# Performance work log

Hardware: AMD Instinct MI355X
Metric: run time of the kernel (lower is better)

## Reference

```python
import jax, jax.numpy as jnp
import numpy as np


def setup_inputs() -> dict:
    key = jax.random.key(0)
    k1, k2, k3 = jax.random.split(key, 3)
    B, H, S, D = 4, 16, 2048, 64
    q = jax.random.normal(k1, (B, H, S, D), dtype=jnp.float32)
    k = jax.random.normal(k2, (B, H, S, D), dtype=jnp.float32)
    v = jax.random.normal(k3, (B, H, S, D), dtype=jnp.float32)
    mask = jnp.ones((B, 1, 1, S), dtype=jnp.int32)  # broadcastable key mask
    return {"q": q, "k": k, "v": v, "mask": mask, "dropout": 0}


def reference(q, k, v, mask, dropout):
    # scores: [B, H, Sq, Sk]
    head_size = q.shape[-1]
    scale = 1.0 / np.sqrt(head_size).astype(np.float32)
    scores = jnp.einsum('bhqd,bhkd->bhqk', q, k) * scale
    scores = jnp.where(mask == 0, jnp.float32(-1e9), scores)
    weights = jax.nn.softmax(scores, axis=-1)
    # dropout is identity in deterministic/eval reference
    values = jnp.einsum('bhqk,bhkd->bhqd', weights, v)
    return values
```

## Files before the change

kernel.cpp:

```cpp
#include <hip/hip_runtime.h>
#include <hip/hip_bf16.h>


#define S_LEN 2048
#define D_DIM 64
#define KVB   64
#define QB    128
#define LDK   72

typedef float  f32x16 __attribute__((ext_vector_type(16)));
typedef __bf16 bf8    __attribute__((ext_vector_type(8)));
typedef __bf16 bf4    __attribute__((ext_vector_type(4)));
typedef __bf16 bf2    __attribute__((ext_vector_type(2)));
typedef unsigned int u32x4 __attribute__((ext_vector_type(4)));

__global__ __launch_bounds__(256, 3)
void sdpa_kernel(const float* __restrict__ q, const float* __restrict__ k,
                 const float* __restrict__ v, const int* __restrict__ mask,
                 float* __restrict__ out) {
    const int bh   = blockIdx.x;
    const int qt   = blockIdx.y;
    const int b    = bh >> 4;
    const int tid  = threadIdx.x;
    const int wave = tid >> 6;
    const int lane = tid & 63;
    const int l31  = lane & 31;
    const int hi   = lane >> 5;

    __shared__ __bf16 Kl[64 * LDK];
    __shared__ __bf16 Vt[64 * LDK];

    const size_t base = (size_t)bh * (S_LEN * D_DIM);

    const int qrow = qt * QB + wave * 32 + l31;
    bf8 qf[4];
    {
        const float* qp = q + base + (size_t)qrow * D_DIM;
        #pragma unroll
        for (int ds = 0; ds < 4; ++ds) {
            float4 a = *(const float4*)(qp + ds * 16 + hi * 8);
            float4 c = *(const float4*)(qp + ds * 16 + hi * 8 + 4);
            bf8 f;
            f[0] = (__bf16)(a.x * 0.125f); f[1] = (__bf16)(a.y * 0.125f);
            f[2] = (__bf16)(a.z * 0.125f); f[3] = (__bf16)(a.w * 0.125f);
            f[4] = (__bf16)(c.x * 0.125f); f[5] = (__bf16)(c.y * 0.125f);
            f[6] = (__bf16)(c.z * 0.125f); f[7] = (__bf16)(c.w * 0.125f);
            qf[ds] = f;
        }
    }

    f32x16 acc0 = (f32x16)0.0f;
    f32x16 acc1 = (f32x16)0.0f;
    float mrun = -INFINITY, lrun = 0.0f;

    for (int kv0 = 0; kv0 < S_LEN; kv0 += KVB) {
        __syncthreads();
        {
            int colg = (tid & 15) * 4;
            int row0 = tid >> 4;
            #pragma unroll
            for (int pp = 0; pp < 4; ++pp) {
                int row = row0 + pp * 16;
                float4 x = *(const float4*)(k + base + (size_t)(kv0 + row) * D_DIM + colg);
                bf4 s;
                s[0] = (__bf16)x.x; s[1] = (__bf16)x.y; s[2] = (__bf16)x.z; s[3] = (__bf16)x.w;
                *(bf4*)(&Kl[row * LDK + colg]) = s;
            }
        }
        {
            int d  = tid & 63;
            int kg = (tid >> 6) * 16;
            __bf16 tmp[16];
            #pragma unroll
            for (int j = 0; j < 16; ++j)
                tmp[j] = (__bf16)v[base + (size_t)(kv0 + kg + j) * D_DIM + d];
            *(bf8*)(&Vt[d * LDK + kg])     = *(bf8*)(&tmp[0]);
            *(bf8*)(&Vt[d * LDK + kg + 8]) = *(bf8*)(&tmp[8]);
        }
        __syncthreads();

        unsigned long long bm = __ballot(mask[b * S_LEN + kv0 + lane] != 0);

        f32x16 p0 = (f32x16)0.0f, p1 = (f32x16)0.0f;
        #pragma unroll
        for (int ds = 0; ds < 4; ++ds) {
            bf8 k0 = *(const bf8*)(&Kl[l31 * LDK        + ds * 16 + hi * 8]);
            bf8 k1 = *(const bf8*)(&Kl[(32 + l31) * LDK + ds * 16 + hi * 8]);
            p0 = __builtin_amdgcn_mfma_f32_32x32x16_bf16(k0, qf[ds], p0, 0, 0, 0);
            p1 = __builtin_amdgcn_mfma_f32_32x32x16_bf16(k1, qf[ds], p1, 0, 0, 0);
        }

        if (bm != ~0ull) {
            #pragma unroll
            for (int r = 0; r < 16; ++r) {
                int kr = (r & 3) + 8 * (r >> 2) + 4 * hi;
                if (!((bm >> kr) & 1))        p0[r] = -1e9f;
                if (!((bm >> (32 + kr)) & 1)) p1[r] = -1e9f;
            }
        }

        float mx = -INFINITY;
        #pragma unroll
        for (int r = 0; r < 16; ++r) mx = fmaxf(mx, fmaxf(p0[r], p1[r]));
        mx = fmaxf(mx, __shfl_xor(mx, 32));
        float mnew = fmaxf(mrun, mx);
        float sc = __expf(mrun - mnew);
        mrun = mnew;
        lrun *= sc;
        #pragma unroll
        for (int r = 0; r < 16; ++r) { acc0[r] *= sc; acc1[r] *= sc; }

        float rs = 0.0f;
        auto do_kb = [&](f32x16& p, int kbbase) {
            #pragma unroll
            for (int r = 0; r < 16; ++r) { p[r] = __expf(p[r] - mnew); rs += p[r]; }
            unsigned wds[8], xw[8];
            #pragma unroll
            for (int j = 0; j < 8; ++j) {
                bf2 t; t[0] = (__bf16)p[2 * j]; t[1] = (__bf16)p[2 * j + 1];
                wds[j] = __builtin_bit_cast(unsigned, t);
            }
            #pragma unroll
            for (int j = 0; j < 8; ++j)
                xw[j] = (unsigned)__shfl_xor((int)wds[j], 32);
            #pragma unroll
            for (int ks = 0; ks < 2; ++ks) {
                u32x4 uu;
                uu[0] = hi ? xw[4 * ks + 2]  : wds[4 * ks + 0];
                uu[1] = hi ? xw[4 * ks + 3]  : wds[4 * ks + 1];
                uu[2] = hi ? wds[4 * ks + 2] : xw[4 * ks + 0];
                uu[3] = hi ? wds[4 * ks + 3] : xw[4 * ks + 1];
                bf8 pf = __builtin_bit_cast(bf8, uu);
                bf8 v0 = *(const bf8*)(&Vt[l31 * LDK        + kbbase + ks * 16 + hi * 8]);
                bf8 v1 = *(const bf8*)(&Vt[(32 + l31) * LDK + kbbase + ks * 16 + hi * 8]);
                acc0 = __builtin_amdgcn_mfma_f32_32x32x16_bf16(v0, pf, acc0, 0, 0, 0);
                acc1 = __builtin_amdgcn_mfma_f32_32x32x16_bf16(v1, pf, acc1, 0, 0, 0);
            }
        };
        do_kb(p0, 0);
        do_kb(p1, 32);
        rs += __shfl_xor(rs, 32);
        lrun += rs;
    }

    float inv = 1.0f / lrun;
    float* op = out + base + (size_t)qrow * D_DIM;
    #pragma unroll
    for (int g = 0; g < 4; ++g) {
        int d0 = g * 8 + hi * 4;
        float4 s0, s1;
        s0.x = acc0[4 * g + 0] * inv; s0.y = acc0[4 * g + 1] * inv;
        s0.z = acc0[4 * g + 2] * inv; s0.w = acc0[4 * g + 3] * inv;
        s1.x = acc1[4 * g + 0] * inv; s1.y = acc1[4 * g + 1] * inv;
        s1.z = acc1[4 * g + 2] * inv; s1.w = acc1[4 * g + 3] * inv;
        *(float4*)(op + d0)      = s0;
        *(float4*)(op + 32 + d0) = s1;
    }
}

extern "C" void kernel_launch(void* const* d_in, const int* in_sizes, int n_in,
                              void* d_out, int out_size, void* d_ws, size_t ws_size,
                              hipStream_t stream) {
    (void)in_sizes; (void)n_in; (void)d_ws; (void)ws_size; (void)out_size;
    const float* q    = (const float*)d_in[0];
    const float* k    = (const float*)d_in[1];
    const float* v    = (const float*)d_in[2];
    const int*   mask = (const int*)d_in[3];
    float* out = (float*)d_out;

    dim3 grid(64, 16);
    dim3 block(256);
    sdpa_kernel<<<grid, block, 0, stream>>>(q, k, v, mask, out);
}
```

Before: 262.6 us.

## Prefetch next K/V tile into registers and use lazy exp2 softmax rescaling

Global loads for the next K/V tile are issued into registers before the current tile's MFMA and softmax work, then converted and written to LDS after that compute, so memory latency overlaps with math. Softmax switches to base-2 exponentials with log2(e) folded into the Q scale. Accumulator rescaling is skipped unless some lane's running max grows by more than 8. The max and sum reductions are restructured as trees to shorten dependency chains. This raises register pressure from the staged K/V values and relies on a bounded-overflow argument for the lazy rescale.

```diff
diff --git a/kernel.cpp b/kernel.cpp
--- a/kernel.cpp
+++ b/kernel.cpp
@@ -13,6 +13,8 @@
 typedef __bf16 bf4    __attribute__((ext_vector_type(4)));
 typedef __bf16 bf2    __attribute__((ext_vector_type(2)));
 typedef unsigned int u32x4 __attribute__((ext_vector_type(4)));
+
+#define QSCALE (0.125f * 1.44269504088896340736f)
 
 __global__ __launch_bounds__(256, 3)
 void sdpa_kernel(const float* __restrict__ q, const float* __restrict__ k,
@@ -32,6 +34,39 @@
 
     const size_t base = (size_t)bh * (S_LEN * D_DIM);
 
+    const int colg = (tid & 15) * 4;
+    const int row0 = tid >> 4;
+    const int dd   = tid & 63;
+    const int kg   = (tid >> 6) * 16;
+
+    float4 kx[4];
+    float  vx[16];
+
+    auto load_regs = [&](int kv0) {
+        const float* kp = k + base + (size_t)(kv0 + row0) * D_DIM + colg;
+        #pragma unroll
+        for (int p = 0; p < 4; ++p)
+            kx[p] = *(const float4*)(kp + (size_t)p * 16 * D_DIM);
+        const float* vp = v + base + (size_t)(kv0 + kg) * D_DIM + dd;
+        #pragma unroll
+        for (int j = 0; j < 16; ++j)
+            vx[j] = vp[(size_t)j * D_DIM];
+    };
+    auto store_lds = [&]() {
+        #pragma unroll
+        for (int p = 0; p < 4; ++p) {
+            bf4 s;
+            s[0] = (__bf16)kx[p].x; s[1] = (__bf16)kx[p].y;
+            s[2] = (__bf16)kx[p].z; s[3] = (__bf16)kx[p].w;
+            *(bf4*)(&Kl[(row0 + p * 16) * LDK + colg]) = s;
+        }
+        __bf16 tmp[16];
+        #pragma unroll
+        for (int j = 0; j < 16; ++j) tmp[j] = (__bf16)vx[j];
+        *(bf8*)(&Vt[dd * LDK + kg])     = *(bf8*)(&tmp[0]);
+        *(bf8*)(&Vt[dd * LDK + kg + 8]) = *(bf8*)(&tmp[8]);
+    };
+
     const int qrow = qt * QB + wave * 32 + l31;
     bf8 qf[4];
     {
@@ -41,10 +76,10 @@
             float4 a = *(const float4*)(qp + ds * 16 + hi * 8);
             float4 c = *(const float4*)(qp + ds * 16 + hi * 8 + 4);
             bf8 f;
-            f[0] = (__bf16)(a.x * 0.125f); f[1] = (__bf16)(a.y * 0.125f);
-            f[2] = (__bf16)(a.z * 0.125f); f[3] = (__bf16)(a.w * 0.125f);
-            f[4] = (__bf16)(c.x * 0.125f); f[5] = (__bf16)(c.y * 0.125f);
-            f[6] = (__bf16)(c.z * 0.125f); f[7] = (__bf16)(c.w * 0.125f);
+            f[0] = (__bf16)(a.x * QSCALE); f[1] = (__bf16)(a.y * QSCALE);
+            f[2] = (__bf16)(a.z * QSCALE); f[3] = (__bf16)(a.w * QSCALE);
+            f[4] = (__bf16)(c.x * QSCALE); f[5] = (__bf16)(c.y * QSCALE);
+            f[6] = (__bf16)(c.z * QSCALE); f[7] = (__bf16)(c.w * QSCALE);
             qf[ds] = f;
         }
     }
@@ -53,33 +88,16 @@
     f32x16 acc1 = (f32x16)0.0f;
     float mrun = -INFINITY, lrun = 0.0f;
 
+    load_regs(0);
+    store_lds();
+    __syncthreads();
+
     for (int kv0 = 0; kv0 < S_LEN; kv0 += KVB) {
-        __syncthreads();
-        {
-            int colg = (tid & 15) * 4;
-            int row0 = tid >> 4;
-            #pragma unroll
-            for (int pp = 0; pp < 4; ++pp) {
-                int row = row0 + pp * 16;
-                float4 x = *(const float4*)(k + base + (size_t)(kv0 + row) * D_DIM + colg);
-                bf4 s;
-                s[0] = (__bf16)x.x; s[1] = (__bf16)x.y; s[2] = (__bf16)x.z; s[3] = (__bf16)x.w;
-                *(bf4*)(&Kl[row * LDK + colg]) = s;
-            }
-        }
-        {
-            int d  = tid & 63;
-            int kg = (tid >> 6) * 16;
-            __bf16 tmp[16];
-            #pragma unroll
-            for (int j = 0; j < 16; ++j)
-                tmp[j] = (__bf16)v[base + (size_t)(kv0 + kg + j) * D_DIM + d];
-            *(bf8*)(&Vt[d * LDK + kg])     = *(bf8*)(&tmp[0]);
-            *(bf8*)(&Vt[d * LDK + kg + 8]) = *(bf8*)(&tmp[8]);
-        }
-        __syncthreads();
-
-        unsigned long long bm = __ballot(mask[b * S_LEN + kv0 + lane] != 0);
+        const bool more = (kv0 + KVB < S_LEN);
+
+        int mk = mask[b * S_LEN + kv0 + lane];
+        if (more) load_regs(kv0 + KVB);
+        unsigned long long bm = __ballot(mk != 0);
 
         f32x16 p0 = (f32x16)0.0f, p1 = (f32x16)0.0f;
         #pragma unroll
@@ -99,21 +117,32 @@
             }
         }
 
-        float mx = -INFINITY;
-        #pragma unroll
-        for (int r = 0; r < 16; ++r) mx = fmaxf(mx, fmaxf(p0[r], p1[r]));
+        float tt[16];
+        #pragma unroll
+        for (int r = 0; r < 16; ++r) tt[r] = fmaxf(p0[r], p1[r]);
+        #pragma unroll
+        for (int r = 0; r < 8; ++r) tt[r] = fmaxf(tt[r], tt[r + 8]);
+        #pragma unroll
+        for (int r = 0; r < 4; ++r) tt[r] = fmaxf(tt[r], tt[r + 4]);
+        float mx = fmaxf(fmaxf(tt[0], tt[1]), fmaxf(tt[2], tt[3]));
         mx = fmaxf(mx, __shfl_xor(mx, 32));
-        float mnew = fmaxf(mrun, mx);
-        float sc = __expf(mrun - mnew);
-        mrun = mnew;
-        lrun *= sc;
-        #pragma unroll
-        for (int r = 0; r < 16; ++r) { acc0[r] *= sc; acc1[r] *= sc; }
-
-        float rs = 0.0f;
+
+        if (!__all(mx - mrun <= 8.0f)) {
+            float mnew = fmaxf(mrun, mx);
+            float sc = __builtin_amdgcn_exp2f(mrun - mnew);
+            lrun *= sc;
+            #pragma unroll
+            for (int r = 0; r < 16; ++r) { acc0[r] *= sc; acc1[r] *= sc; }
+            mrun = mnew;
+        }
+
+        float rsp[4] = {0.0f, 0.0f, 0.0f, 0.0f};
         auto do_kb = [&](f32x16& p, int kbbase) {
             #pragma unroll
-            for (int r = 0; r < 16; ++r) { p[r] = __expf(p[r] - mnew); rs += p[r]; }
+            for (int r = 0; r < 16; ++r) {
+                p[r] = __builtin_amdgcn_exp2f(p[r] - mrun);
+                rsp[r & 3] += p[r];
+            }
             unsigned wds[8], xw[8];
             #pragma unroll
             for (int j = 0; j < 8; ++j) {
@@ -139,8 +168,15 @@
         };
         do_kb(p0, 0);
         do_kb(p1, 32);
+        float rs = (rsp[0] + rsp[1]) + (rsp[2] + rsp[3]);
         rs += __shfl_xor(rs, 32);
         lrun += rs;
+
+        if (more) {
+            __syncthreads();
+            store_lds();
+            __syncthreads();
+        }
     }
 
     float inv = 1.0f / lrun;
```

Result: slower. 283.2 us (+7.8%).
